# Kernel optimization log

Hardware: AMD Instinct MI355X
Metric: run time of the kernel (lower is better)

Reference implementation:

```python
import jax, jax.numpy as jnp
import numpy as np

EPS = 1e-08
B, P = 16, 2048


def setup_inputs() -> dict:
    key = jax.random.key(0)
    k1, k2, k3, k4, k5 = jax.random.split(key, 5)
    return {
        "R_t": jax.random.normal(k1, (B, 3, 3), dtype=jnp.float32),
        "t_t": jax.random.normal(k2, (B, 3), dtype=jnp.float32),
        "R_prev": jax.random.normal(k3, (B, 3, 3), dtype=jnp.float32),
        "t_prev": jax.random.normal(k4, (B, 3), dtype=jnp.float32),
        "model_points": jax.random.normal(k5, (B, P, 3), dtype=jnp.float32),
    }


def reference(R_t, t_t, R_prev, t_prev, model_points):
    # Transform CAD points by each pose: pts = points @ R^T + t
    pts_t = jnp.einsum("bpj,bij->bpi", model_points, R_t) + t_t[:, None, :]       # (B,P,3)
    pts_prev = jnp.einsum("bpj,bij->bpi", model_points, R_prev) + t_prev[:, None, :]
    # Pairwise L2 distances (same math as torch: diff -> sumsq -> sqrt(.+eps))
    diff = pts_t[:, :, None, :] - pts_prev[:, None, :, :]                          # (B,P,P,3)
    pairwise_dist = jnp.sqrt(jnp.sum(diff * diff, axis=-1) + EPS)                  # (B,P,P)
    min_t_to_prev = jnp.min(pairwise_dist, axis=2)                                 # (B,P)
    min_prev_to_t = jnp.min(pairwise_dist, axis=1)                                 # (B,P)
    loss_per_sample = jnp.mean(min_t_to_prev, axis=1) + jnp.mean(min_prev_to_t, axis=1)
    return jnp.mean(loss_per_sample)
```

## Files before the change

kernel.cpp:

```cpp
#include <hip/hip_runtime.h>
#include <math.h>

#define BB 16
#define PP 2048
#define EPSF 1e-8f
#define SCALE (1.0f / (BB * PP))
#define NCHUNK 32
#define CHUNK 64
#define RPT 8

__global__ __launch_bounds__(256) void pairtrans_kernel(
    const float* __restrict__ R_t, const float* __restrict__ t_t,
    const float* __restrict__ R_p, const float* __restrict__ t_p,
    const float* __restrict__ mp,
    float* __restrict__ partial, float* __restrict__ out) {
  __shared__ float4 tile[CHUNK];
  int blk = blockIdx.x;
  int t = threadIdx.x;
  if (blk == 0 && t == 0) *out = 0.0f;
  int cc = blk & 31;
  int db = blk >> 5;
  int dir = db & 1;
  int b = db >> 1;
  const float* Rr = (dir ? R_p : R_t) + b * 9;
  const float* tr_ = (dir ? t_p : t_t) + b * 3;
  const float* Rc = (dir ? R_t : R_p) + b * 9;
  const float* tc_ = (dir ? t_t : t_p) + b * 3;

  if (t < CHUNK) {
    int ci = (b << 11) + (cc << 6) + t;
    float x = mp[ci * 3], y = mp[ci * 3 + 1], z = mp[ci * 3 + 2];
    float qx = fmaf(Rc[0], x, fmaf(Rc[1], y, fmaf(Rc[2], z, tc_[0])));
    float qy = fmaf(Rc[3], x, fmaf(Rc[4], y, fmaf(Rc[5], z, tc_[1])));
    float qz = fmaf(Rc[6], x, fmaf(Rc[7], y, fmaf(Rc[8], z, tc_[2])));
    float qw = fmaf(qx, qx, fmaf(qy, qy, qz * qz));
    tile[t] = make_float4(-2.f * qx, -2.f * qy, -2.f * qz, qw);
  }

  float r0 = Rr[0], r1 = Rr[1], r2 = Rr[2], r3 = Rr[3], r4 = Rr[4],
        r5 = Rr[5], r6 = Rr[6], r7 = Rr[7], r8 = Rr[8];
  float t0 = tr_[0], t1 = tr_[1], t2 = tr_[2];
  float4 a[RPT];
#pragma unroll
  for (int k = 0; k < RPT; ++k) {
    int ri = (b << 11) + (k << 8) + t;
    float x = mp[ri * 3], y = mp[ri * 3 + 1], z = mp[ri * 3 + 2];
    float px = fmaf(r0, x, fmaf(r1, y, fmaf(r2, z, t0)));
    float py = fmaf(r3, x, fmaf(r4, y, fmaf(r5, z, t1)));
    float pz = fmaf(r6, x, fmaf(r7, y, fmaf(r8, z, t2)));
    a[k] = make_float4(px, py, pz, fmaf(px, px, fmaf(py, py, pz * pz)));
  }
  __syncthreads();

  float m[RPT];
#pragma unroll
  for (int k = 0; k < RPT; ++k) m[k] = 3.0e38f;

#pragma unroll 4
  for (int j = 0; j < CHUNK; j += 2) {
    float4 q0 = tile[j];
    float4 q1 = tile[j + 1];
#pragma unroll
    for (int k = 0; k < RPT; ++k) {
      float s0 = fmaf(a[k].x, q0.x, fmaf(a[k].y, q0.y, fmaf(a[k].z, q0.z, q0.w)));
      float s1 = fmaf(a[k].x, q1.x, fmaf(a[k].y, q1.y, fmaf(a[k].z, q1.z, q1.w)));
      m[k] = fminf(fminf(m[k], s0), s1);
    }
  }

  float* pp = partial + (cc << 16) + (db << 11) + t;
#pragma unroll
  for (int k = 0; k < RPT; ++k) pp[k << 8] = m[k] + a[k].w;
}

__global__ __launch_bounds__(256) void finish_kernel(
    const float* __restrict__ partial, float* __restrict__ out) {
  int idx = blockIdx.x * 256 + threadIdx.x;
  float v = partial[idx];
#pragma unroll
  for (int c = 1; c < NCHUNK; ++c) v = fminf(v, partial[(c << 16) + idx]);
  v = fmaxf(v, 0.0f);
  float s = sqrtf(v + EPSF) * SCALE;
  for (int off = 32; off; off >>= 1) s += __shfl_down(s, off, 64);
  __shared__ float wsum[4];
  if ((threadIdx.x & 63) == 0) wsum[threadIdx.x >> 6] = s;
  __syncthreads();
  if (threadIdx.x == 0) atomicAdd(out, wsum[0] + wsum[1] + wsum[2] + wsum[3]);
}

__global__ __launch_bounds__(256) void fallback_kernel(
    const float* __restrict__ R_t, const float* __restrict__ t_t,
    const float* __restrict__ R_p, const float* __restrict__ t_p,
    const float* __restrict__ mp, float* __restrict__ out) {
  __shared__ float4 lds[PP];
  int blk = blockIdx.x;
  int rc  = blk & 7;
  int dir = (blk >> 3) & 1;
  int b   = blk >> 4;
  const float* Rr = (dir ? R_p : R_t) + b * 9;
  const float* tr_ = (dir ? t_p : t_t) + b * 3;
  const float* Rc = (dir ? R_t : R_p) + b * 9;
  const float* tcp = (dir ? t_t : t_p) + b * 3;
  float c0 = Rc[0], c1 = Rc[1], c2 = Rc[2], c3 = Rc[3], c4 = Rc[4],
        c5 = Rc[5], c6 = Rc[6], c7 = Rc[7], c8 = Rc[8];
  float tc0 = tcp[0], tc1 = tcp[1], tc2 = tcp[2];
  for (int j = threadIdx.x; j < PP; j += 256) {
    int gi = (b * PP + j) * 3;
    float x = mp[gi], y = mp[gi + 1], z = mp[gi + 2];
    float4 q;
    q.x = fmaf(c0, x, fmaf(c1, y, fmaf(c2, z, tc0)));
    q.y = fmaf(c3, x, fmaf(c4, y, fmaf(c5, z, tc1)));
    q.z = fmaf(c6, x, fmaf(c7, y, fmaf(c8, z, tc2)));
    q.w = 0.f;
    lds[j] = q;
  }
  __syncthreads();
  int row = rc * 256 + threadIdx.x;
  int gi = (b * PP + row) * 3;
  float x = mp[gi], y = mp[gi + 1], z = mp[gi + 2];
  float ax = fmaf(Rr[0], x, fmaf(Rr[1], y, fmaf(Rr[2], z, tr_[0])));
  float ay = fmaf(Rr[3], x, fmaf(Rr[4], y, fmaf(Rr[5], z, tr_[1])));
  float az = fmaf(Rr[6], x, fmaf(Rr[7], y, fmaf(Rr[8], z, tr_[2])));
  float m = 3.4e38f;
#pragma unroll 8
  for (int j = 0; j < PP; ++j) {
    float4 q = lds[j];
    float dx = ax - q.x, dy = ay - q.y, dz = az - q.z;
    float d = fmaf(dx, dx, fmaf(dy, dy, dz * dz));
    m = fminf(m, d);
  }
  float v = sqrtf(m + EPSF) * SCALE;
  for (int off = 32; off; off >>= 1) v += __shfl_down(v, off, 64);
  __shared__ float wsum[4];
  if ((threadIdx.x & 63) == 0) wsum[threadIdx.x >> 6] = v;
  __syncthreads();
  if (threadIdx.x == 0) atomicAdd(out, wsum[0] + wsum[1] + wsum[2] + wsum[3]);
}

extern "C" void kernel_launch(void* const* d_in, const int* in_sizes, int n_in,
                              void* d_out, int out_size, void* d_ws, size_t ws_size,
                              hipStream_t stream) {
  const float* R_t = (const float*)d_in[0];
  const float* t_t = (const float*)d_in[1];
  const float* R_p = (const float*)d_in[2];
  const float* t_p = (const float*)d_in[3];
  const float* mp  = (const float*)d_in[4];
  float* out = (float*)d_out;

  size_t need = (size_t)NCHUNK * 2 * BB * PP * sizeof(float);
  if (ws_size >= need) {
    float* partial = (float*)d_ws;
    pairtrans_kernel<<<1024, 256, 0, stream>>>(R_t, t_t, R_p, t_p, mp, partial, out);
    finish_kernel<<<256, 256, 0, stream>>>(partial, out);
  } else {
    hipMemsetAsync(d_out, 0, sizeof(float), stream);
    fallback_kernel<<<256, 256, 0, stream>>>(R_t, t_t, R_p, t_p, mp, out);
  }
}
```

Measured before the change: 25.61 us.

## Use packed FP32 FMA with SoA LDS tiles and 16 rows per thread

```diff
diff --git a/kernel.cpp b/kernel.cpp
--- a/kernel.cpp
+++ b/kernel.cpp
@@ -6,49 +6,67 @@
 #define EPSF 1e-8f
 #define SCALE (1.0f / (BB * PP))
 #define NCHUNK 32
-#define CHUNK 64
-#define RPT 8
+#define RPT 16
+
+typedef float f2 __attribute__((ext_vector_type(2)));
+
+static __device__ __forceinline__ f2 pkfma(f2 a, f2 b, f2 c) {
+  f2 d;
+  asm("v_pk_fma_f32 %0, %1, %2, %3" : "=v"(d) : "v"(a), "v"(b), "v"(c));
+  return d;
+}
 
 __global__ __launch_bounds__(256) void pairtrans_kernel(
     const float* __restrict__ R_t, const float* __restrict__ t_t,
     const float* __restrict__ R_p, const float* __restrict__ t_p,
     const float* __restrict__ mp,
     float* __restrict__ partial, float* __restrict__ out) {
-  __shared__ float4 tile[CHUNK];
+  __shared__ f2 Qx[2][32], Qy[2][32], Qz[2][32], Qw[2][32];
   int blk = blockIdx.x;
   int t = threadIdx.x;
   if (blk == 0 && t == 0) *out = 0.0f;
-  int cc = blk & 31;
-  int db = blk >> 5;
+  int sc = blk & 15;
+  int db = blk >> 4;
   int dir = db & 1;
   int b = db >> 1;
+  int h = t >> 7;
+  int tl = t & 127;
+  int cc = (sc << 1) | h;
   const float* Rr = (dir ? R_p : R_t) + b * 9;
   const float* tr_ = (dir ? t_p : t_t) + b * 3;
   const float* Rc = (dir ? R_t : R_p) + b * 9;
   const float* tc_ = (dir ? t_t : t_p) + b * 3;
 
-  if (t < CHUNK) {
-    int ci = (b << 11) + (cc << 6) + t;
+  if (tl < 64) {
+    int ci = (b << 11) + (cc << 6) + tl;
     float x = mp[ci * 3], y = mp[ci * 3 + 1], z = mp[ci * 3 + 2];
     float qx = fmaf(Rc[0], x, fmaf(Rc[1], y, fmaf(Rc[2], z, tc_[0])));
     float qy = fmaf(Rc[3], x, fmaf(Rc[4], y, fmaf(Rc[5], z, tc_[1])));
     float qz = fmaf(Rc[6], x, fmaf(Rc[7], y, fmaf(Rc[8], z, tc_[2])));
     float qw = fmaf(qx, qx, fmaf(qy, qy, qz * qz));
-    tile[t] = make_float4(-2.f * qx, -2.f * qy, -2.f * qz, qw);
+    ((float*)&Qx[h][0])[tl] = -2.f * qx;
+    ((float*)&Qy[h][0])[tl] = -2.f * qy;
+    ((float*)&Qz[h][0])[tl] = -2.f * qz;
+    ((float*)&Qw[h][0])[tl] = qw;
   }
 
   float r0 = Rr[0], r1 = Rr[1], r2 = Rr[2], r3 = Rr[3], r4 = Rr[4],
         r5 = Rr[5], r6 = Rr[6], r7 = Rr[7], r8 = Rr[8];
   float t0 = tr_[0], t1 = tr_[1], t2 = tr_[2];
-  float4 a[RPT];
+  f2 ax[RPT / 2], ay[RPT / 2], az[RPT / 2], aw[RPT / 2];
 #pragma unroll
   for (int k = 0; k < RPT; ++k) {
-    int ri = (b << 11) + (k << 8) + t;
+    int ri = (b << 11) + (k << 7) + tl;
     float x = mp[ri * 3], y = mp[ri * 3 + 1], z = mp[ri * 3 + 2];
     float px = fmaf(r0, x, fmaf(r1, y, fmaf(r2, z, t0)));
     float py = fmaf(r3, x, fmaf(r4, y, fmaf(r5, z, t1)));
     float pz = fmaf(r6, x, fmaf(r7, y, fmaf(r8, z, t2)));
-    a[k] = make_float4(px, py, pz, fmaf(px, px, fmaf(py, py, pz * pz)));
+    float pw = fmaf(px, px, fmaf(py, py, pz * pz));
+    if (k & 1) {
+      ax[k >> 1].y = px; ay[k >> 1].y = py; az[k >> 1].y = pz; aw[k >> 1].y = pw;
+    } else {
+      ax[k >> 1].x = px; ay[k >> 1].x = py; az[k >> 1].x = pz; aw[k >> 1].x = pw;
+    }
   }
   __syncthreads();
 
@@ -56,21 +74,34 @@
 #pragma unroll
   for (int k = 0; k < RPT; ++k) m[k] = 3.0e38f;
 
-#pragma unroll 4
-  for (int j = 0; j < CHUNK; j += 2) {
-    float4 q0 = tile[j];
-    float4 q1 = tile[j + 1];
+  const f2* qx = &Qx[h][0];
+  const f2* qy = &Qy[h][0];
+  const f2* qz = &Qz[h][0];
+  const f2* qw = &Qw[h][0];
+
+#pragma unroll 2
+  for (int jp = 0; jp < 32; ++jp) {
+    f2 X = qx[jp], Y = qy[jp], Z = qz[jp], W = qw[jp];
+    f2 Xs, Ys, Zs, Ws;
+    Xs.x = X.y; Xs.y = X.x;
+    Ys.x = Y.y; Ys.y = Y.x;
+    Zs.x = Z.y; Zs.y = Z.x;
+    Ws.x = W.y; Ws.y = W.x;
 #pragma unroll
-    for (int k = 0; k < RPT; ++k) {
-      float s0 = fmaf(a[k].x, q0.x, fmaf(a[k].y, q0.y, fmaf(a[k].z, q0.z, q0.w)));
-      float s1 = fmaf(a[k].x, q1.x, fmaf(a[k].y, q1.y, fmaf(a[k].z, q1.z, q1.w)));
-      m[k] = fminf(fminf(m[k], s0), s1);
+    for (int kk = 0; kk < RPT / 2; ++kk) {
+      f2 d1 = pkfma(ax[kk], X, pkfma(ay[kk], Y, pkfma(az[kk], Z, W)));
+      f2 d2 = pkfma(ax[kk], Xs, pkfma(ay[kk], Ys, pkfma(az[kk], Zs, Ws)));
+      m[2 * kk]     = fminf(fminf(m[2 * kk], d1.x), d2.x);
+      m[2 * kk + 1] = fminf(fminf(m[2 * kk + 1], d1.y), d2.y);
     }
   }
 
-  float* pp = partial + (cc << 16) + (db << 11) + t;
+  float* pp = partial + (cc << 16) + (db << 11) + tl;
 #pragma unroll
-  for (int k = 0; k < RPT; ++k) pp[k << 8] = m[k] + a[k].w;
+  for (int kk = 0; kk < RPT / 2; ++kk) {
+    pp[(2 * kk) << 7]     = m[2 * kk] + aw[kk].x;
+    pp[(2 * kk + 1) << 7] = m[2 * kk + 1] + aw[kk].y;
+  }
 }
 
 __global__ __launch_bounds__(256) void finish_kernel(
@@ -150,7 +181,7 @@
   size_t need = (size_t)NCHUNK * 2 * BB * PP * sizeof(float);
   if (ws_size >= need) {
     float* partial = (float*)d_ws;
-    pairtrans_kernel<<<1024, 256, 0, stream>>>(R_t, t_t, R_p, t_p, mp, partial, out);
+    pairtrans_kernel<<<512, 256, 0, stream>>>(R_t, t_t, R_p, t_p, mp, partial, out);
     finish_kernel<<<256, 256, 0, stream>>>(partial, out);
   } else {
     hipMemsetAsync(d_out, 0, sizeof(float), stream);
```

Result: no change. 25.35 us (-1.0%).
